# Kernel optimization log

Measured on AMD Instinct MI355X. Metric: run time of the kernel, lower is better.

The kernel has to match this reference:

```python
import jax, jax.numpy as jnp
import numpy as np

N_NODES = 50000
N_EDGES = 800000
D = 64
E_DIM = 2
C = 8


def _spline_basis(pseudo, K):
    """Open B-spline basis, degree=1. pseudo: [Ne, E] in [0,1).
    Returns basis B [Ne, S] and flat weight index WI [Ne, S], S = 2**E."""
    E = pseudo.shape[1]
    v = pseudo * (K - 1)
    lo_f = jnp.floor(v)
    frac = v - lo_f
    lo = lo_f.astype(jnp.int32)
    idx = jnp.stack([jnp.clip(lo, 0, K - 1), jnp.clip(lo + 1, 0, K - 1)], axis=-1)  # [Ne,E,2]
    bas = jnp.stack([1.0 - frac, frac], axis=-1)                                   # [Ne,E,2]
    combos = jnp.asarray(
        np.stack(np.meshgrid(*([np.arange(2)] * E), indexing='ij'), -1).reshape(-1, E)
    )  # [S,E]
    d_idx = jnp.arange(E)[None, :]          # broadcast to [S,E]
    B = jnp.prod(bas[:, d_idx, combos], axis=-1)  # [Ne,S]
    stride = (K ** jnp.arange(E)).astype(jnp.int32)  # [E]
    WI = jnp.sum(idx[:, d_idx, combos] * stride[None, None, :], axis=-1)  # [Ne,S]
    return B, WI


def _spline_conv(x, src, dst, pseudo, W, root, bias, K, num_nodes):
    """SplineConv (degree=1, open spline, aggr='mean', root_weight, bias).
    x: [N,Din], W: [K**E, Din, Dout], root: [Din, Dout]."""
    B, WI = _spline_basis(pseudo, K)                 # [Ne,S], [Ne,S]
    Y = jnp.einsum('nd,kdo->nko', x, W)              # [N, K**E, Dout]
    gathered = Y[src[:, None], WI]                   # [Ne, S, Dout]
    m = jnp.einsum('es,eso->eo', B, gathered)        # [Ne, Dout]
    msum = jax.ops.segment_sum(m, dst, num_segments=num_nodes)
    cnt = jax.ops.segment_sum(jnp.ones((m.shape[0], 1), m.dtype), dst, num_segments=num_nodes)
    aggr = msum / jnp.maximum(cnt, 1.0)
    return aggr + x @ root + bias


def setup_inputs() -> dict:
    key = jax.random.key(0)
    ks = jax.random.split(key, 16)
    s = 1.0 / np.sqrt(D)
    return {
        'x': jax.random.normal(ks[0], (N_NODES, D), jnp.float32),
        'edge_index': jax.random.randint(ks[1], (2, N_EDGES), 0, N_NODES, jnp.int32),
        'edge_attr': jax.random.uniform(ks[2], (N_EDGES, E_DIM), jnp.float32),
        'W1': jax.random.normal(ks[3], (3 ** E_DIM, D, D), jnp.float32) * s,
        'root1': jax.random.normal(ks[4], (D, D), jnp.float32) * s,
        'b1': jax.random.normal(ks[5], (D,), jnp.float32) * 0.01,
        'W2': jax.random.normal(ks[6], (5 ** E_DIM, D, D), jnp.float32) * s,
        'root2': jax.random.normal(ks[7], (D, D), jnp.float32) * s,
        'b2': jax.random.normal(ks[8], (D,), jnp.float32) * 0.01,
        'mlp1_w': jax.random.normal(ks[9], (D, D), jnp.float32) * s,
        'mlp1_b': jax.random.normal(ks[10], (D,), jnp.float32) * 0.01,
        'mlp2_w': jax.random.normal(ks[11], (D, C), jnp.float32) * s,
        'mlp2_b': jax.random.normal(ks[12], (C,), jnp.float32) * 0.01,
    }


def reference(x, edge_index, edge_attr, W1, root1, b1, W2, root2, b2,
              mlp1_w, mlp1_b, mlp2_w, mlp2_b):
    N = x.shape[0]
    src, dst = edge_index[0], edge_index[1]
    h = jax.nn.elu(_spline_conv(x, src, dst, edge_attr, W1, root1, b1, 3, N))
    # dropout is identity in eval mode
    h = jax.nn.elu(_spline_conv(h, src, dst, edge_attr, W2, root2, b2, 5, N))
    # task='node', G=0 -> no pooling / no concat
    h = jax.nn.relu(h @ mlp1_w + mlp1_b)
    h = jax.nn.relu(h @ mlp2_w + mlp2_b)
    return h
```

## Files before the change

### kernel.cpp

```cpp
#include <hip/hip_runtime.h>
#include <hip/hip_bf16.h>

typedef __attribute__((ext_vector_type(8))) short short8;
typedef __attribute__((ext_vector_type(4))) short short4v;
typedef __attribute__((ext_vector_type(4))) unsigned int uint4v;
typedef __attribute__((ext_vector_type(4))) float floatx4;
typedef __attribute__((ext_vector_type(16))) float floatx16;

__device__ __forceinline__ unsigned short f2bf(float x) {
  __hip_bfloat16 h = __float2bfloat16(x);
  return __builtin_bit_cast(unsigned short, h);
}
__device__ __forceinline__ float bf2f(unsigned short u) {
  return __builtin_bit_cast(float, (unsigned int)u << 16);
}
__device__ __forceinline__ unsigned int pk_bf16(float lo, float hi) {
  return ((unsigned int)f2bf(hi) << 16) | (unsigned int)f2bf(lo);
}

__global__ __launch_bounds__(256) void cvt_x_kernel(
    const float4* __restrict__ X, unsigned short* __restrict__ Xbf, int n4) {
  int i = blockIdx.x * 256 + threadIdx.x;
  if (i < n4) {
    float4 v = X[i];
    short4v o = {(short)f2bf(v.x), (short)f2bf(v.y),
                 (short)f2bf(v.z), (short)f2bf(v.w)};
    *(short4v*)&Xbf[i * 4] = o;
  }
}

__global__ __launch_bounds__(256) void pack_b_kernel(
    const float* __restrict__ W, const float* __restrict__ root,
    unsigned short* __restrict__ Bpk, int K2) {
  int R = (K2 + 1) * 64;
  int total = 64 * R;
  int i = blockIdx.x * 256 + threadIdx.x;
  if (i >= total) return;
  int j = i & 7;
  int lane = (i >> 3) & 63;
  int rest = i >> 9;
  int wv = rest & 3, kc = rest >> 2;
  int o = wv * 16 + (lane & 15);
  int p = kc * 32 + ((lane >> 4) & 3) * 8 + j;
  int k = p >> 6, q6 = p & 63;
  float v = (k < K2) ? W[(k << 12) + (q6 << 6) + o] : root[(q6 << 6) + o];
  Bpk[i] = f2bf(v);
}

__global__ __launch_bounds__(256) void zero_int_kernel(int* __restrict__ p, int n) {
  int i = blockIdx.x * 256 + threadIdx.x;
  if (i < n) p[i] = 0;
}

__global__ __launch_bounds__(256) void hist_kernel(
    const int* __restrict__ dst, int* __restrict__ deg, int nE) {
  int e = blockIdx.x * 256 + threadIdx.x;
  if (e < nE) atomicAdd(&deg[dst[e]], 1);
}

__global__ __launch_bounds__(256) void blocksum_kernel(
    const int* __restrict__ deg, int* __restrict__ partial, int N) {
  __shared__ int s[256];
  int t = threadIdx.x, i = blockIdx.x * 256 + t;
  s[t] = (i < N) ? deg[i] : 0;
  __syncthreads();
  for (int off = 128; off > 0; off >>= 1) {
    if (t < off) s[t] += s[t + off];
    __syncthreads();
  }
  if (t == 0) partial[blockIdx.x] = s[0];
}

__global__ __launch_bounds__(256) void scanpartials_kernel(
    int* __restrict__ partial, int nb) {
  __shared__ int s[256];
  int t = threadIdx.x;
  int v = (t < nb) ? partial[t] : 0;
  s[t] = v;
  __syncthreads();
  for (int off = 1; off < 256; off <<= 1) {
    int x = (t >= off) ? s[t - off] : 0;
    __syncthreads();
    s[t] += x;
    __syncthreads();
  }
  if (t < nb) partial[t] = s[t] - v;
}

__global__ __launch_bounds__(256) void blockscan_kernel(
    const int* __restrict__ deg, const int* __restrict__ partial,
    int* __restrict__ row_start, int* __restrict__ cursor, int N, int nE) {
  __shared__ int s[256];
  int t = threadIdx.x, i = blockIdx.x * 256 + t;
  int v = (i < N) ? deg[i] : 0;
  s[t] = v;
  __syncthreads();
  for (int off = 1; off < 256; off <<= 1) {
    int x = (t >= off) ? s[t - off] : 0;
    __syncthreads();
    s[t] += x;
    __syncthreads();
  }
  if (i < N) {
    int excl = s[t] - v + partial[blockIdx.x];
    row_start[i] = excl;
    cursor[i] = excl;
  }
  if (i == 0) row_start[N] = nE;
}

__global__ __launch_bounds__(256) void scatter_rec_kernel(
    const int* __restrict__ dst, const int* __restrict__ src,
    const float* __restrict__ attr, int* __restrict__ cursor,
    float4* __restrict__ recS, int nE) {
  int e = blockIdx.x * 256 + threadIdx.x;
  if (e < 16) recS[nE + e] = make_float4(0.f, 0.f, 0.f, 0.f);
  if (e >= nE) return;
  int pos = atomicAdd(&cursor[dst[e]], 1);
  float2 a = *(const float2*)&attr[2 * e];
  recS[pos] = make_float4(a.x * 4.f, a.y * 4.f,
                          __builtin_bit_cast(float, src[e] * 64), 0.f);
}

template <int K, int K2, int OUTBF, int NODES, int GRP, int MINW>
__global__ __launch_bounds__(256, MINW) void spline_layer_kernel(
    const float4* __restrict__ rec, const int* __restrict__ row_start,
    const unsigned short* __restrict__ Xbf, const unsigned short* __restrict__ Bpk,
    const float* __restrict__ bias, void* __restrict__ outv, int N, float uscale) {
  constexpr int RZ = K2 * 64;
  constexpr int AS = RZ + 8;
  constexpr int NKZ = RZ / 32;
  constexpr int NKC = (K2 + 1) * 2;
  constexpr int GN = NODES / 4;
  __shared__ unsigned short As[NODES * AS];
  __shared__ __align__(16) float invs[16];
  const int t = threadIdx.x, w = t >> 6, lane = t & 63;
  const int nodeBase = blockIdx.x * NODES;

  const int col = lane & 31, half = lane >> 5, col2 = col * 2;
  const float mi0f = (col < K2) ? (float)(col % K) : -1e9f;
  const float mi1f = (col < K2) ? (float)(col / K) : 0.f;

  if constexpr (NODES < 16) {
    if (w == 3 && lane >= 60) invs[lane - 48] = 1.0f;
  }

  for (int g = 0; g < GN; ++g) {
    const int row = w * GN + g;
    const int node = nodeBase + row;
    if (node < N) {
      floatx16 d0, d1;
#pragma unroll
      for (int i = 0; i < 16; ++i) { d0[i] = 0.f; d1[i] = 0.f; }

      const int beg = row_start[node], end = row_start[node + 1];
      if (lane == 0) invs[row] = 1.f / (float)max(end - beg, 1);
      for (int c0 = beg; c0 < end; c0 += 16) {
        const int ib = c0 + half * 8;
        const int rem = end - ib;
        float4 rj[8];
#pragma unroll
        for (int j = 0; j < 8; ++j) rj[j] = rec[ib + j];
        short8 A;
        unsigned int xv[8];
#pragma unroll
        for (int j = 0; j < 8; ++j) {
          float t0 = fmaf(rj[j].x, -uscale, mi0f);
          float t1 = fmaf(rj[j].y, -uscale, mi1f);
          float su = fmaxf(0.f, 1.f - fabsf(t0));
          float sv = fmaxf(0.f, 1.f - fabsf(t1));
          float p = (j < rem) ? su * sv : 0.f;
          A[j] = (short)f2bf(p);
          xv[j] = *(const unsigned int*)(Xbf +
                    (__builtin_bit_cast(int, rj[j].z) + col2));
        }
        uint4v blo, bhi;
#pragma unroll
        for (int i = 0; i < 4; ++i) {
          blo[i] = __builtin_amdgcn_perm(xv[2 * i + 1], xv[2 * i], 0x05040100u);
          bhi[i] = __builtin_amdgcn_perm(xv[2 * i + 1], xv[2 * i], 0x07060302u);
        }
        d0 = __builtin_amdgcn_mfma_f32_32x32x16_bf16(
                 A, __builtin_bit_cast(short8, blo), d0, 0, 0, 0);
        d1 = __builtin_amdgcn_mfma_f32_32x32x16_bf16(
                 A, __builtin_bit_cast(short8, bhi), d1, 0, 0, 0);
      }

#pragma unroll
      for (int reg = 0; reg < 16; ++reg) {
        int r = (reg & 3) + 8 * (reg >> 2) + 4 * half;
        if (r < K2)
          *(unsigned int*)&As[row * AS + r * 64 + col2] =
              pk_bf16(d0[reg], d1[reg]);
      }
    } else {
      if (lane == 0) invs[row] = 1.0f;
      for (int i = lane; i < RZ / 2; i += 64)
        ((unsigned int*)&As[row * AS])[i] = 0;
    }
  }
  __syncthreads();

  const int mrow = lane & 15, q = lane >> 4;
  const int arow = (NODES < 16) ? min(mrow, NODES - 1) : mrow;
  const int anode = min(nodeBase + arow, N - 1);
  floatx4 aZ0 = {0.f, 0.f, 0.f, 0.f};
  floatx4 aZ1 = {0.f, 0.f, 0.f, 0.f};
  floatx4 aR  = {0.f, 0.f, 0.f, 0.f};
#pragma unroll
  for (int kc0 = 0; kc0 < NKC; kc0 += GRP) {
    short8 av[GRP], bv[GRP];
#pragma unroll
    for (int u = 0; u < GRP; ++u) {
      const int kc = kc0 + u;
      if (kc < NKZ)
        av[u] = *(const short8*)&As[arow * AS + kc * 32 + q * 8];
      else
        av[u] = *(const short8*)&Xbf[(size_t)anode * 64 + (kc - NKZ) * 32 + q * 8];
      bv[u] = *(const short8*)&Bpk[(((size_t)kc * 4 + w) * 64 + lane) * 8];
    }
#pragma unroll
    for (int u = 0; u < GRP; ++u) {
      const int kc = kc0 + u;
      if (kc >= NKZ)
        aR = __builtin_amdgcn_mfma_f32_16x16x32_bf16(av[u], bv[u], aR, 0, 0, 0);
      else if ((kc0 / GRP) & 1)
        aZ1 = __builtin_amdgcn_mfma_f32_16x16x32_bf16(av[u], bv[u], aZ1, 0, 0, 0);
      else
        aZ0 = __builtin_amdgcn_mfma_f32_16x16x32_bf16(av[u], bv[u], aZ0, 0, 0, 0);
    }
  }

  const int o = w * 16 + mrow;
  const float bvs = bias[o];
  const floatx4 invv = *(const floatx4*)&invs[q * 4];
#pragma unroll
  for (int reg = 0; reg < 4; ++reg) {
    int rloc = q * 4 + reg;
    int node = nodeBase + rloc;
    if (rloc < NODES && node < N) {
      float v = (aZ0[reg] + aZ1[reg]) * invv[reg] + aR[reg] + bvs;
      v = v > 0.f ? v : (expf(v) - 1.f);
      if (OUTBF)
        ((unsigned short*)outv)[(size_t)node * 64 + o] = f2bf(v);
      else
        ((float*)outv)[(size_t)node * 64 + o] = v;
    }
  }
}

__global__ __launch_bounds__(256) void head_kernel(
    const unsigned short* __restrict__ h2bf, const unsigned short* __restrict__ m1pk,
    const float* __restrict__ m1b, const float* __restrict__ m2w,
    const float* __restrict__ m2b, float* __restrict__ out, int N) {
  __shared__ unsigned short Hs[64 * 72];
  __shared__ unsigned short Ts[64 * 72];
  __shared__ float W2s[512];
  const int t = threadIdx.x, w = t >> 6, lane = t & 63;
  const int n0 = blockIdx.x * 64;

  for (int i = t; i < 512; i += 256) {
    int row = i >> 3, cg = i & 7;
    int n = n0 + row;
    floatx4 val = {0.f, 0.f, 0.f, 0.f};
    if (n < N) val = *(const floatx4*)&h2bf[(size_t)n * 64 + cg * 8];
    *(floatx4*)&Hs[row * 72 + cg * 8] = val;
  }
  for (int i = t; i < 512; i += 256) W2s[i] = m2w[i];
  __syncthreads();

  const int mrow = lane & 15, q = lane >> 4;
  const int o = w * 16 + mrow;
  const float bv = m1b[o];
#pragma unroll
  for (int rg = 0; rg < 4; ++rg) {
    floatx4 acc = {0.f, 0.f, 0.f, 0.f};
#pragma unroll
    for (int kc = 0; kc < 2; ++kc) {
      short8 a = *(const short8*)&Hs[(rg * 16 + mrow) * 72 + kc * 32 + q * 8];
      short8 b = *(const short8*)&m1pk[(((size_t)kc * 4 + w) * 64 + lane) * 8];
      acc = __builtin_amdgcn_mfma_f32_16x16x32_bf16(a, b, acc, 0, 0, 0);
    }
#pragma unroll
    for (int reg = 0; reg < 4; ++reg) {
      int row = rg * 16 + q * 4 + reg;
      float v = acc[reg] + bv;
      Ts[row * 72 + o] = f2bf(v > 0.f ? v : 0.f);
    }
  }
  __syncthreads();

  for (int i = t; i < 512; i += 256) {
    int nl = i >> 3, c = i & 7;
    int n = n0 + nl;
    if (n >= N) continue;
    float s = m2b[c];
    for (int d = 0; d < 64; ++d) s += bf2f(Ts[nl * 72 + d]) * W2s[d * 8 + c];
    out[(size_t)n * 8 + c] = s > 0.f ? s : 0.f;
  }
}

extern "C" void kernel_launch(void* const* d_in, const int* in_sizes, int n_in,
                              void* d_out, int out_size, void* d_ws, size_t ws_size,
                              hipStream_t stream) {
  const float* x     = (const float*)d_in[0];
  const int*   ei    = (const int*)d_in[1];
  const float* attr  = (const float*)d_in[2];
  const float* W1    = (const float*)d_in[3];
  const float* root1 = (const float*)d_in[4];
  const float* b1    = (const float*)d_in[5];
  const float* W2    = (const float*)d_in[6];
  const float* root2 = (const float*)d_in[7];
  const float* b2    = (const float*)d_in[8];
  const float* m1w   = (const float*)d_in[9];
  const float* m1b   = (const float*)d_in[10];
  const float* m2w   = (const float*)d_in[11];
  const float* m2b   = (const float*)d_in[12];

  const int N  = in_sizes[0] / 64;
  const int nE = in_sizes[1] / 2;
  const int* src  = ei;
  const int* dstv = ei + nE;
  float* out = (float*)d_out;

  int* deg       = (int*)d_ws;
  int* row_start = deg + N;
  int* cursor    = row_start + (N + 1);
  int* partial   = cursor + N;
  char* pbase = (char*)(partial + 256);
  pbase = (char*)(((uintptr_t)pbase + 15) & ~(uintptr_t)15);
  float4* recS = (float4*)pbase;
  unsigned short* Xbf  = (unsigned short*)(recS + nE + 16);
  unsigned short* h1bf = Xbf + (size_t)N * 64;
  unsigned short* h2bf = h1bf + (size_t)N * 64;
  unsigned short* Bpk1 = h2bf + (size_t)N * 64;
  unsigned short* Bpk2 = Bpk1 + 64 * 640;
  unsigned short* m1pk = Bpk2 + 64 * 1664;

  dim3 blk(256);
  int nbN  = (N + 255) / 256;
  int nbE  = (nE + 255) / 256;
  int nbF1 = (N + 15) / 16;
  int nbF2 = (N + 11) / 12;
  int nbH  = (N + 63) / 64;

  zero_int_kernel<<<nbN, blk, 0, stream>>>(deg, N);
  hist_kernel<<<nbE, blk, 0, stream>>>(dstv, deg, nE);
  blocksum_kernel<<<nbN, blk, 0, stream>>>(deg, partial, N);
  scanpartials_kernel<<<1, blk, 0, stream>>>(partial, nbN);
  blockscan_kernel<<<nbN, blk, 0, stream>>>(deg, partial, row_start, cursor, N, nE);
  scatter_rec_kernel<<<nbE, blk, 0, stream>>>(dstv, src, attr, cursor, recS, nE);

  pack_b_kernel<<<(64 * 640 + 255) / 256, blk, 0, stream>>>(W1, root1, Bpk1, 9);
  pack_b_kernel<<<(64 * 1664 + 255) / 256, blk, 0, stream>>>(W2, root2, Bpk2, 25);
  pack_b_kernel<<<(64 * 64 + 255) / 256, blk, 0, stream>>>(m1w, m1w, m1pk, 0);
  cvt_x_kernel<<<(N * 16 + 255) / 256, blk, 0, stream>>>(
      (const float4*)x, Xbf, N * 16);

  spline_layer_kernel<3, 9, 1, 16, 4, 6><<<nbF1, blk, 0, stream>>>(
      recS, row_start, Xbf, Bpk1, b1, h1bf, N, 0.5f);

  spline_layer_kernel<5, 25, 1, 12, 4, 4><<<nbF2, blk, 0, stream>>>(
      recS, row_start, h1bf, Bpk2, b2, h2bf, N, 1.0f);

  head_kernel<<<nbH, blk, 0, stream>>>(h2bf, m1pk, m1b, m2w, m2b, out, N);
}
```

Baseline: 315.0 us.

## Sort nodes by degree class and prefetch edge records in spline layers

Nodes are bucketed into 16-edge degree classes with atomics and processed in that permuted order, so each block's waves see similar chunk counts and less load imbalance. Layer 2 software-prefetches the next chunk's edge records while gathering features, and the tail masking is skipped on full chunks. Layer 1's minimum-waves launch bound rises from 6 to 8. The cost is extra atomics during the scan, an indirection through the permutation, and scattered output writes.

```diff
diff --git a/kernel.cpp b/kernel.cpp
--- a/kernel.cpp
+++ b/kernel.cpp
@@ -59,10 +59,16 @@
 }
 
 __global__ __launch_bounds__(256) void blocksum_kernel(
-    const int* __restrict__ deg, int* __restrict__ partial, int N) {
+    const int* __restrict__ deg, int* __restrict__ partial,
+    int* __restrict__ clsCnt, int N) {
   __shared__ int s[256];
   int t = threadIdx.x, i = blockIdx.x * 256 + t;
-  s[t] = (i < N) ? deg[i] : 0;
+  int v = (i < N) ? deg[i] : 0;
+  s[t] = v;
+  if (i < N) {
+    int c = min((v + 15) >> 4, 7);
+    atomicAdd(&clsCnt[c], 1);
+  }
   __syncthreads();
   for (int off = 128; off > 0; off >>= 1) {
     if (t < off) s[t] += s[t + off];
@@ -72,7 +78,8 @@
 }
 
 __global__ __launch_bounds__(256) void scanpartials_kernel(
-    int* __restrict__ partial, int nb) {
+    int* __restrict__ partial, int nb,
+    const int* __restrict__ clsCnt, int* __restrict__ clsCur) {
   __shared__ int s[256];
   int t = threadIdx.x;
   int v = (t < nb) ? partial[t] : 0;
@@ -85,11 +92,16 @@
     __syncthreads();
   }
   if (t < nb) partial[t] = s[t] - v;
+  if (t == 0) {
+    int acc = 0;
+    for (int c = 0; c < 8; ++c) { clsCur[c] = acc; acc += clsCnt[c]; }
+  }
 }
 
 __global__ __launch_bounds__(256) void blockscan_kernel(
     const int* __restrict__ deg, const int* __restrict__ partial,
-    int* __restrict__ row_start, int* __restrict__ cursor, int N, int nE) {
+    int* __restrict__ row_start, int* __restrict__ cursor, int N, int nE,
+    int* __restrict__ clsCur, int* __restrict__ perm) {
   __shared__ int s[256];
   int t = threadIdx.x, i = blockIdx.x * 256 + t;
   int v = (i < N) ? deg[i] : 0;
@@ -105,6 +117,9 @@
     int excl = s[t] - v + partial[blockIdx.x];
     row_start[i] = excl;
     cursor[i] = excl;
+    int c = min((v + 15) >> 4, 7);
+    int p = atomicAdd(&clsCur[c], 1);
+    perm[p] = i;
   }
   if (i == 0) row_start[N] = nE;
 }
@@ -114,7 +129,7 @@
     const float* __restrict__ attr, int* __restrict__ cursor,
     float4* __restrict__ recS, int nE) {
   int e = blockIdx.x * 256 + threadIdx.x;
-  if (e < 16) recS[nE + e] = make_float4(0.f, 0.f, 0.f, 0.f);
+  if (e < 32) recS[nE + e] = make_float4(0.f, 0.f, 0.f, 0.f);
   if (e >= nE) return;
   int pos = atomicAdd(&cursor[dst[e]], 1);
   float2 a = *(const float2*)&attr[2 * e];
@@ -122,9 +137,10 @@
                           __builtin_bit_cast(float, src[e] * 64), 0.f);
 }
 
-template <int K, int K2, int OUTBF, int NODES, int GRP, int MINW>
+template <int K, int K2, int OUTBF, int NODES, int GRP, int MINW, int PF>
 __global__ __launch_bounds__(256, MINW) void spline_layer_kernel(
     const float4* __restrict__ rec, const int* __restrict__ row_start,
+    const int* __restrict__ perm,
     const unsigned short* __restrict__ Xbf, const unsigned short* __restrict__ Bpk,
     const float* __restrict__ bias, void* __restrict__ outv, int N, float uscale) {
   constexpr int RZ = K2 * 64;
@@ -134,6 +150,7 @@
   constexpr int GN = NODES / 4;
   __shared__ unsigned short As[NODES * AS];
   __shared__ __align__(16) float invs[16];
+  __shared__ int pnode[16];
   const int t = threadIdx.x, w = t >> 6, lane = t & 63;
   const int nodeBase = blockIdx.x * NODES;
 
@@ -141,38 +158,64 @@
   const float mi0f = (col < K2) ? (float)(col % K) : -1e9f;
   const float mi1f = (col < K2) ? (float)(col / K) : 0.f;
 
+  if (t < NODES) {
+    int pidx = nodeBase + t;
+    pnode[t] = (pidx < N) ? perm[pidx] : 0;
+  }
   if constexpr (NODES < 16) {
     if (w == 3 && lane >= 60) invs[lane - 48] = 1.0f;
   }
+  __syncthreads();
 
   for (int g = 0; g < GN; ++g) {
     const int row = w * GN + g;
-    const int node = nodeBase + row;
-    if (node < N) {
+    if (nodeBase + row < N) {
+      const int node = pnode[row];
       floatx16 d0, d1;
 #pragma unroll
       for (int i = 0; i < 16; ++i) { d0[i] = 0.f; d1[i] = 0.f; }
 
       const int beg = row_start[node], end = row_start[node + 1];
       if (lane == 0) invs[row] = 1.f / (float)max(end - beg, 1);
+
+      float4 rjn[8];
+      if constexpr (PF) {
+        const int ib0 = beg + half * 8;
+#pragma unroll
+        for (int j = 0; j < 8; ++j) rjn[j] = rec[ib0 + j];
+      }
       for (int c0 = beg; c0 < end; c0 += 16) {
-        const int ib = c0 + half * 8;
-        const int rem = end - ib;
         float4 rj[8];
-#pragma unroll
-        for (int j = 0; j < 8; ++j) rj[j] = rec[ib + j];
+        if constexpr (PF) {
+#pragma unroll
+          for (int j = 0; j < 8; ++j) rj[j] = rjn[j];
+        } else {
+          const int ib = c0 + half * 8;
+#pragma unroll
+          for (int j = 0; j < 8; ++j) rj[j] = rec[ib + j];
+        }
+        unsigned int xv[8];
+#pragma unroll
+        for (int j = 0; j < 8; ++j)
+          xv[j] = *(const unsigned int*)(Xbf +
+                    (__builtin_bit_cast(int, rj[j].z) + col2));
+        if constexpr (PF) {
+          const int ibn = c0 + 16 + half * 8;
+#pragma unroll
+          for (int j = 0; j < 8; ++j) rjn[j] = rec[ibn + j];
+        }
         short8 A;
-        unsigned int xv[8];
+        const bool fullc = (end - c0 >= 16);
+        const int rem = end - (c0 + half * 8);
 #pragma unroll
         for (int j = 0; j < 8; ++j) {
           float t0 = fmaf(rj[j].x, -uscale, mi0f);
           float t1 = fmaf(rj[j].y, -uscale, mi1f);
           float su = fmaxf(0.f, 1.f - fabsf(t0));
           float sv = fmaxf(0.f, 1.f - fabsf(t1));
-          float p = (j < rem) ? su * sv : 0.f;
+          float p = su * sv;
+          if (!fullc) p = (j < rem) ? p : 0.f;
           A[j] = (short)f2bf(p);
-          xv[j] = *(const unsigned int*)(Xbf +
-                    (__builtin_bit_cast(int, rj[j].z) + col2));
         }
         uint4v blo, bhi;
 #pragma unroll
@@ -203,7 +246,7 @@
 
   const int mrow = lane & 15, q = lane >> 4;
   const int arow = (NODES < 16) ? min(mrow, NODES - 1) : mrow;
-  const int anode = min(nodeBase + arow, N - 1);
+  const int anode = pnode[arow];
   floatx4 aZ0 = {0.f, 0.f, 0.f, 0.f};
   floatx4 aZ1 = {0.f, 0.f, 0.f, 0.f};
   floatx4 aR  = {0.f, 0.f, 0.f, 0.f};
@@ -237,8 +280,8 @@
 #pragma unroll
   for (int reg = 0; reg < 4; ++reg) {
     int rloc = q * 4 + reg;
-    int node = nodeBase + rloc;
-    if (rloc < NODES && node < N) {
+    if (rloc < NODES && nodeBase + rloc < N) {
+      int node = pnode[rloc];
       float v = (aZ0[reg] + aZ1[reg]) * invv[reg] + aR[reg] + bvs;
       v = v > 0.f ? v : (expf(v) - 1.f);
       if (OUTBF)
@@ -324,13 +367,16 @@
   float* out = (float*)d_out;
 
   int* deg       = (int*)d_ws;
-  int* row_start = deg + N;
+  int* clsCnt    = deg + N;
+  int* clsCur    = clsCnt + 8;
+  int* row_start = clsCur + 8;
   int* cursor    = row_start + (N + 1);
   int* partial   = cursor + N;
-  char* pbase = (char*)(partial + 256);
+  int* perm      = partial + 256;
+  char* pbase = (char*)(perm + N);
   pbase = (char*)(((uintptr_t)pbase + 15) & ~(uintptr_t)15);
   float4* recS = (float4*)pbase;
-  unsigned short* Xbf  = (unsigned short*)(recS + nE + 16);
+  unsigned short* Xbf  = (unsigned short*)(recS + nE + 32);
   unsigned short* h1bf = Xbf + (size_t)N * 64;
   unsigned short* h2bf = h1bf + (size_t)N * 64;
   unsigned short* Bpk1 = h2bf + (size_t)N * 64;
@@ -344,11 +390,12 @@
   int nbF2 = (N + 11) / 12;
   int nbH  = (N + 63) / 64;
 
-  zero_int_kernel<<<nbN, blk, 0, stream>>>(deg, N);
+  zero_int_kernel<<<nbN, blk, 0, stream>>>(deg, N + 16);
   hist_kernel<<<nbE, blk, 0, stream>>>(dstv, deg, nE);
-  blocksum_kernel<<<nbN, blk, 0, stream>>>(deg, partial, N);
-  scanpartials_kernel<<<1, blk, 0, stream>>>(partial, nbN);
-  blockscan_kernel<<<nbN, blk, 0, stream>>>(deg, partial, row_start, cursor, N, nE);
+  blocksum_kernel<<<nbN, blk, 0, stream>>>(deg, partial, clsCnt, N);
+  scanpartials_kernel<<<1, blk, 0, stream>>>(partial, nbN, clsCnt, clsCur);
+  blockscan_kernel<<<nbN, blk, 0, stream>>>(deg, partial, row_start, cursor,
+                                            N, nE, clsCur, perm);
   scatter_rec_kernel<<<nbE, blk, 0, stream>>>(dstv, src, attr, cursor, recS, nE);
 
   pack_b_kernel<<<(64 * 640 + 255) / 256, blk, 0, stream>>>(W1, root1, Bpk1, 9);
@@ -357,11 +404,11 @@
   cvt_x_kernel<<<(N * 16 + 255) / 256, blk, 0, stream>>>(
       (const float4*)x, Xbf, N * 16);
 
-  spline_layer_kernel<3, 9, 1, 16, 4, 6><<<nbF1, blk, 0, stream>>>(
-      recS, row_start, Xbf, Bpk1, b1, h1bf, N, 0.5f);
-
-  spline_layer_kernel<5, 25, 1, 12, 4, 4><<<nbF2, blk, 0, stream>>>(
-      recS, row_start, h1bf, Bpk2, b2, h2bf, N, 1.0f);
+  spline_layer_kernel<3, 9, 1, 16, 4, 8, 0><<<nbF1, blk, 0, stream>>>(
+      recS, row_start, perm, Xbf, Bpk1, b1, h1bf, N, 0.5f);
+
+  spline_layer_kernel<5, 25, 1, 12, 4, 4, 1><<<nbF2, blk, 0, stream>>>(
+      recS, row_start, perm, h1bf, Bpk2, b2, h2bf, N, 1.0f);
 
   head_kernel<<<nbH, blk, 0, stream>>>(h2bf, m1pk, m1b, m2w, m2b, out, N);
 }
```

Result: slower. 1.226 ms (+289.4%).

## Balance node rows across waves dynamically and prefetch edge records in layer two

Applied to the files above, without the earlier changes.

Static per-wave row assignment in the spline layer kernel is replaced by a shared atomic work counter, so waves take node rows dynamically and degree imbalance across rows evens out. A compile-time PF option software-prefetches the next chunk of 16 edge records while the current chunk's gathers and MFMAs run; it is enabled only for the second layer. The gathered-X loads are now issued before the basis computation, and the per-edge tail mask is skipped for full chunks. The record padding grows to 32 so the prefetch can read past the last chunk safely. Layer one's occupancy hint drops from 6 to 4, and the prefetch raises register pressure.

```diff
diff --git a/kernel.cpp b/kernel.cpp
--- a/kernel.cpp
+++ b/kernel.cpp
@@ -114,7 +114,7 @@
     const float* __restrict__ attr, int* __restrict__ cursor,
     float4* __restrict__ recS, int nE) {
   int e = blockIdx.x * 256 + threadIdx.x;
-  if (e < 16) recS[nE + e] = make_float4(0.f, 0.f, 0.f, 0.f);
+  if (e < 32) recS[nE + e] = make_float4(0.f, 0.f, 0.f, 0.f);
   if (e >= nE) return;
   int pos = atomicAdd(&cursor[dst[e]], 1);
   float2 a = *(const float2*)&attr[2 * e];
@@ -122,7 +122,7 @@
                           __builtin_bit_cast(float, src[e] * 64), 0.f);
 }
 
-template <int K, int K2, int OUTBF, int NODES, int GRP, int MINW>
+template <int K, int K2, int OUTBF, int NODES, int GRP, int MINW, int PF>
 __global__ __launch_bounds__(256, MINW) void spline_layer_kernel(
     const float4* __restrict__ rec, const int* __restrict__ row_start,
     const unsigned short* __restrict__ Xbf, const unsigned short* __restrict__ Bpk,
@@ -131,9 +131,9 @@
   constexpr int AS = RZ + 8;
   constexpr int NKZ = RZ / 32;
   constexpr int NKC = (K2 + 1) * 2;
-  constexpr int GN = NODES / 4;
   __shared__ unsigned short As[NODES * AS];
   __shared__ __align__(16) float invs[16];
+  __shared__ int wcur;
   const int t = threadIdx.x, w = t >> 6, lane = t & 63;
   const int nodeBase = blockIdx.x * NODES;
 
@@ -141,12 +141,16 @@
   const float mi0f = (col < K2) ? (float)(col % K) : -1e9f;
   const float mi1f = (col < K2) ? (float)(col / K) : 0.f;
 
+  if (t == 0) wcur = 0;
   if constexpr (NODES < 16) {
     if (w == 3 && lane >= 60) invs[lane - 48] = 1.0f;
   }
-
-  for (int g = 0; g < GN; ++g) {
-    const int row = w * GN + g;
+  __syncthreads();
+
+  int row;
+  if (lane == 0) row = atomicAdd(&wcur, 1);
+  row = __shfl(row, 0);
+  while (row < NODES) {
     const int node = nodeBase + row;
     if (node < N) {
       floatx16 d0, d1;
@@ -155,24 +159,45 @@
 
       const int beg = row_start[node], end = row_start[node + 1];
       if (lane == 0) invs[row] = 1.f / (float)max(end - beg, 1);
+
+      float4 rjn[8];
+      if constexpr (PF) {
+        const int ib0 = beg + half * 8;
+#pragma unroll
+        for (int j = 0; j < 8; ++j) rjn[j] = rec[ib0 + j];
+      }
       for (int c0 = beg; c0 < end; c0 += 16) {
-        const int ib = c0 + half * 8;
-        const int rem = end - ib;
         float4 rj[8];
-#pragma unroll
-        for (int j = 0; j < 8; ++j) rj[j] = rec[ib + j];
+        if constexpr (PF) {
+#pragma unroll
+          for (int j = 0; j < 8; ++j) rj[j] = rjn[j];
+        } else {
+          const int ib = c0 + half * 8;
+#pragma unroll
+          for (int j = 0; j < 8; ++j) rj[j] = rec[ib + j];
+        }
+        unsigned int xv[8];
+#pragma unroll
+        for (int j = 0; j < 8; ++j)
+          xv[j] = *(const unsigned int*)(Xbf +
+                    (__builtin_bit_cast(int, rj[j].z) + col2));
+        if constexpr (PF) {
+          const int ibn = c0 + 16 + half * 8;
+#pragma unroll
+          for (int j = 0; j < 8; ++j) rjn[j] = rec[ibn + j];
+        }
         short8 A;
-        unsigned int xv[8];
+        const bool fullc = (end - c0 >= 16);
+        const int rem = end - (c0 + half * 8);
 #pragma unroll
         for (int j = 0; j < 8; ++j) {
           float t0 = fmaf(rj[j].x, -uscale, mi0f);
           float t1 = fmaf(rj[j].y, -uscale, mi1f);
           float su = fmaxf(0.f, 1.f - fabsf(t0));
           float sv = fmaxf(0.f, 1.f - fabsf(t1));
-          float p = (j < rem) ? su * sv : 0.f;
+          float p = su * sv;
+          if (!fullc) p = (j < rem) ? p : 0.f;
           A[j] = (short)f2bf(p);
-          xv[j] = *(const unsigned int*)(Xbf +
-                    (__builtin_bit_cast(int, rj[j].z) + col2));
         }
         uint4v blo, bhi;
 #pragma unroll
@@ -198,6 +223,8 @@
       for (int i = lane; i < RZ / 2; i += 64)
         ((unsigned int*)&As[row * AS])[i] = 0;
     }
+    if (lane == 0) row = atomicAdd(&wcur, 1);
+    row = __shfl(row, 0);
   }
   __syncthreads();
 
@@ -330,7 +357,7 @@
   char* pbase = (char*)(partial + 256);
   pbase = (char*)(((uintptr_t)pbase + 15) & ~(uintptr_t)15);
   float4* recS = (float4*)pbase;
-  unsigned short* Xbf  = (unsigned short*)(recS + nE + 16);
+  unsigned short* Xbf  = (unsigned short*)(recS + nE + 32);
   unsigned short* h1bf = Xbf + (size_t)N * 64;
   unsigned short* h2bf = h1bf + (size_t)N * 64;
   unsigned short* Bpk1 = h2bf + (size_t)N * 64;
@@ -357,10 +384,10 @@
   cvt_x_kernel<<<(N * 16 + 255) / 256, blk, 0, stream>>>(
       (const float4*)x, Xbf, N * 16);
 
-  spline_layer_kernel<3, 9, 1, 16, 4, 6><<<nbF1, blk, 0, stream>>>(
+  spline_layer_kernel<3, 9, 1, 16, 4, 4, 0><<<nbF1, blk, 0, stream>>>(
       recS, row_start, Xbf, Bpk1, b1, h1bf, N, 0.5f);
 
-  spline_layer_kernel<5, 25, 1, 12, 4, 4><<<nbF2, blk, 0, stream>>>(
+  spline_layer_kernel<5, 25, 1, 12, 4, 4, 1><<<nbF2, blk, 0, stream>>>(
       recS, row_start, h1bf, Bpk2, b2, h2bf, N, 1.0f);
 
   head_kernel<<<nbH, blk, 0, stream>>>(h2bf, m1pk, m1b, m2w, m2b, out, N);
```

After: 310.9 us. Within noise of the previous version (-1.3%).
